# Performance work log

Hardware: AMD Instinct MI355X
Metric: run time of the kernel (lower is better)

The kernel has to match this reference:

```python
import jax, jax.numpy as jnp
import numpy as np

NPOINT, NSAMPLE, RADIUS = 2048, 32, 0.2
EPS = 1e-5


def setup_inputs() -> dict:
    key = jax.random.key(0)
    ks = jax.random.split(key, 12)
    B, N, C = 8, 8192, 64
    mlp = [64, 64, 128]
    inp = {
        "xyz": jax.random.normal(ks[0], (B, 3, N), dtype=jnp.float32),
        "points": jax.random.normal(ks[1], (B, C, N), dtype=jnp.float32),
    }
    last = C + 3  # use_xyz concatenates 3 relative coords
    for i, out in enumerate(mlp, 1):
        inp[f"W{i}"] = jax.random.normal(ks[2 * i], (out, last), dtype=jnp.float32) / np.sqrt(last).astype(np.float32)
        inp[f"b{i}"] = jnp.zeros((out,), jnp.float32)
        inp[f"g{i}"] = jnp.ones((out,), jnp.float32)
        inp[f"be{i}"] = jnp.zeros((out,), jnp.float32)
        last = out
    return inp


def fps(xyz_t, npoint):
    """Farthest point sampling. xyz_t: (B,N,3) -> (B,npoint) int32 indices."""
    xyz_t = jax.lax.stop_gradient(xyz_t)  # indices are non-differentiable
    B, N, _ = xyz_t.shape

    def step(carry, _):
        dists, far = carry  # (B,N), (B,)
        cent = jnp.take_along_axis(xyz_t, far[:, None, None], axis=1)  # (B,1,3)
        d = jnp.sum((xyz_t - cent) ** 2, axis=-1)
        dists = jnp.minimum(dists, d)
        nf = jnp.argmax(dists, axis=-1).astype(jnp.int32)
        return (dists, nf), far

    init = (jnp.full((B, N), 1e10, xyz_t.dtype), jnp.zeros((B,), jnp.int32))
    _, idxs = jax.lax.scan(step, init, None, length=npoint)
    return jnp.transpose(idxs)  # (B, npoint)


def ball_query(xyz_t, new_xyz_t, radius, nsample):
    """First-nsample-in-radius neighbor indices, padded with first hit.
    xyz_t (B,N,3), new_xyz_t (B,M,3) -> (B,M,nsample) int32."""
    B, N, _ = xyz_t.shape
    # squared distances via gemm to avoid (B,M,N,3) intermediate
    sq = (jnp.sum(new_xyz_t ** 2, -1)[:, :, None]
          + jnp.sum(xyz_t ** 2, -1)[:, None, :]
          - 2.0 * jnp.einsum('bmd,bnd->bmn', new_xyz_t, xyz_t))  # (B,M,N)
    cand = jnp.where(sq < radius * radius, jnp.arange(N, dtype=jnp.int32), N)
    idx = jnp.sort(cand, axis=-1)[:, :, :nsample]  # first k in-radius by index order
    first = idx[:, :, :1]
    first = jnp.where(first == N, 0, first)  # guard empty groups
    idx = jnp.where(idx == N, first, idx)
    return idx


def group(feat, idx):
    """feat (B,C,N), idx (B,M,k) -> (B,C,M,k) gathered neighbor features."""
    return jnp.take_along_axis(feat[:, :, None, :], idx[:, None, :, :], axis=3)


def conv_bn_relu(x, W, b, g, be):
    """Shared 1x1 Conv2d + BatchNorm2d (batch stats, training mode) + ReLU.
    x: (B,C,M,K) -> (B,O,M,K)."""
    y = jnp.einsum('oc,bcmk->bomk', W, x) + b[None, :, None, None]
    mu = jnp.mean(y, axis=(0, 2, 3), keepdims=True)
    var = jnp.var(y, axis=(0, 2, 3), keepdims=True)
    y = (y - mu) * jax.lax.rsqrt(var + EPS)
    y = y * g[None, :, None, None] + be[None, :, None, None]
    return jax.nn.relu(y)


def reference(xyz, points, W1, b1, g1, be1, W2, b2, g2, be2, W3, b3, g3, be3):
    xyz_t = jnp.transpose(xyz, (0, 2, 1))  # (B,N,3)
    fidx = fps(xyz_t, NPOINT)  # (B,M)
    new_xyz = jnp.take_along_axis(xyz, fidx[:, None, :], axis=2)  # (B,3,M)
    idx = ball_query(xyz_t, jnp.transpose(new_xyz, (0, 2, 1)), RADIUS, NSAMPLE)  # (B,M,K)
    grouped_xyz = group(xyz, idx) - new_xyz[:, :, :, None]  # (B,3,M,K) centered
    grouped_pts = group(points, idx)  # (B,f,M,K)
    x = jnp.concatenate([grouped_xyz, grouped_pts], axis=1)  # (B,f+3,M,K)
    x = conv_bn_relu(x, W1, b1, g1, be1)
    x = conv_bn_relu(x, W2, b2, g2, be2)
    x = conv_bn_relu(x, W3, b3, g3, be3)
    new_points = jnp.max(x, axis=3)  # (B,mlp[-1],M)
    return (new_xyz, new_points)
```

## Files before the change

### kernel.cpp

```cpp
#include <hip/hip_runtime.h>

#define BB 8
#define NN 8192
#define MM 2048
#define KK 32
#define NTOT (BB*MM*KK)

#define WS_PTS_T  0
#define WS_XYZN   4194304
#define WS_IDX    5242880
#define WS_GPART  5767168
#define WS_PARAMS 6291456
#define WS_ZMAX   6292480
#define WS_ZMIN   8389632
#define WS_TOTAL  10486784

typedef float v2f __attribute__((ext_vector_type(2)));

__global__ __launch_bounds__(256) void k_transpose(const float* __restrict__ pts,
                                                   float* __restrict__ pts_t){
  __shared__ float tile[64][65];
  int bid = blockIdx.x;
  int b = bid >> 7;
  int n0 = (bid & 127) << 6;
  int tx = threadIdx.x & 63, ty = threadIdx.x >> 6;
  const float* src = pts + (size_t)b*64*NN;
  #pragma unroll
  for (int c = ty; c < 64; c += 4)
    tile[c][tx] = src[(size_t)c*NN + n0 + tx];
  __syncthreads();
  float* dst = pts_t + ((size_t)b*NN + n0)*64;
  #pragma unroll
  for (int r = ty; r < 64; r += 4)
    dst[(size_t)r*64 + tx] = tile[tx][r];
}

__global__ __launch_bounds__(256) void k_xyzn(const float* __restrict__ xyz,
                                              float4* __restrict__ xyzn){
  #pragma clang fp contract(off)
  int i = blockIdx.x*256 + threadIdx.x;
  int b = i >> 13, n = i & 8191;
  const float* p = xyz + (size_t)b*3*NN;
  float x = p[n], y = p[NN+n], z = p[2*NN+n];
  float nrm = (x*x + y*y) + z*z;
  xyzn[i] = make_float4(x, y, z, nrm);
}

#define FPS_DPP_STEP(ctrl, rmask)                                            \
  {                                                                          \
    unsigned int lo_ = (unsigned int)key, hi_ = (unsigned int)(key >> 32);   \
    unsigned int sl_ = (unsigned int)__builtin_amdgcn_update_dpp(            \
        (int)lo_, (int)lo_, (ctrl), (rmask), 0xf, false);                    \
    unsigned int sh_ = (unsigned int)__builtin_amdgcn_update_dpp(            \
        (int)hi_, (int)hi_, (ctrl), (rmask), 0xf, false);                    \
    unsigned long long ok_ = ((unsigned long long)sh_ << 32) | sl_;          \
    if (ok_ > key) key = ok_;                                                \
  }

__global__ __launch_bounds__(512,1) void k_fps(const float* __restrict__ xyz,
                                               float* __restrict__ out_newxyz){
  #pragma clang fp contract(off)
  __shared__ float4 sp4[NN];
  __shared__ unsigned long long swk[2][8];
  int b = blockIdx.x, tid = threadIdx.x;
  const float* xb = xyz + (size_t)b*3*NN;
  int n0 = tid << 4;
  v2f px[8], py[8], pz[8], dd[8];
  const float4* xb4 = (const float4*)xb;
  #pragma unroll
  for (int q = 0; q < 4; ++q){
    float4 X = xb4[(n0>>2) + q];
    float4 Y = xb4[(NN>>2) + (n0>>2) + q];
    float4 Z = xb4[((2*NN)>>2) + (n0>>2) + q];
    px[2*q]   = (v2f){X.x, X.y}; px[2*q+1] = (v2f){X.z, X.w};
    py[2*q]   = (v2f){Y.x, Y.y}; py[2*q+1] = (v2f){Y.z, Y.w};
    pz[2*q]   = (v2f){Z.x, Z.y}; pz[2*q+1] = (v2f){Z.z, Z.w};
    dd[2*q]   = (v2f){1e10f,1e10f}; dd[2*q+1] = (v2f){1e10f,1e10f};
    sp4[n0+4*q+0] = make_float4(X.x, Y.x, Z.x, 0.f);
    sp4[n0+4*q+1] = make_float4(X.y, Y.y, Z.y, 0.f);
    sp4[n0+4*q+2] = make_float4(X.z, Y.z, Z.z, 0.f);
    sp4[n0+4*q+3] = make_float4(X.w, Y.w, Z.w, 0.f);
  }
  __syncthreads();
  float4 c0 = sp4[0];
  float cx = c0.x, cy = c0.y, cz = c0.z;
  float* ob = out_newxyz + (size_t)b*3*MM;
  int lane = tid & 63, wid = tid >> 6;
  for (int s = 0; s < 4; ++s){
    float ox = 0.f, oy = 0.f, oz = 0.f;
    for (int ti = 0; ti < 512; ++ti){
      if (tid == ti){ ox = cx; oy = cy; oz = cz; }
      v2f cvx = (v2f){cx,cx}, cvy = (v2f){cy,cy}, cvz = (v2f){cz,cz};
      v2f bv2 = (v2f){-1.f,-1.f};
      #pragma unroll
      for (int g = 0; g < 8; ++g){
        v2f dx = px[g]-cvx, dy = py[g]-cvy, dz = pz[g]-cvz;
        v2f xx = dx*dx, yy = dy*dy, zz = dz*dz;
        v2f sum = xx + yy;
        v2f d = sum + zz;
        v2f nd = __builtin_elementwise_min(dd[g], d);
        dd[g] = nd;
        bv2 = __builtin_elementwise_max(bv2, nd);
      }
      float bv = fmaxf(bv2.x, bv2.y);
      int bj = 0;
      #pragma unroll
      for (int g = 7; g >= 0; --g){
        if (dd[g].y == bv) bj = 2*g+1;
        if (dd[g].x == bv) bj = 2*g;
      }
      unsigned int n = (unsigned int)(n0 + bj);
      unsigned long long key =
          ((unsigned long long)__float_as_uint(bv) << 32) | (unsigned int)(~n);
      FPS_DPP_STEP(0x111, 0xf)
      FPS_DPP_STEP(0x112, 0xf)
      FPS_DPP_STEP(0x114, 0xf)
      FPS_DPP_STEP(0x118, 0xf)
      FPS_DPP_STEP(0x142, 0xa)
      FPS_DPP_STEP(0x143, 0xc)
      int buf = ti & 1;
      if (lane == 63) swk[buf][wid] = key;
      __syncthreads();
      const unsigned long long* kk = swk[buf];
      unsigned long long k0=kk[0], k1=kk[1], k2=kk[2], k3=kk[3];
      unsigned long long k4=kk[4], k5=kk[5], k6=kk[6], k7=kk[7];
      unsigned long long a = (k0>k1)?k0:k1, c = (k2>k3)?k2:k3;
      unsigned long long e = (k4>k5)?k4:k5, f = (k6>k7)?k6:k7;
      unsigned long long g2 = (a>c)?a:c,   h2 = (e>f)?e:f;
      unsigned long long kmax = (g2>h2)?g2:h2;
      int far = (int)(~(unsigned int)kmax) & (NN-1);
      float4 c4 = sp4[far];
      cx = c4.x; cy = c4.y; cz = c4.z;
    }
    ob[(s<<9)+tid] = ox; ob[MM+(s<<9)+tid] = oy; ob[2*MM+(s<<9)+tid] = oz;
  }
}

__global__ __launch_bounds__(256) void k_ballq(const float4* __restrict__ xyzn,
                                               const float* __restrict__ newxyz,
                                               int* __restrict__ idx){
  #pragma clang fp contract(off)
  __shared__ unsigned long long s_mask[32][129];
  __shared__ float4 s_c4[32];
  const float R2 = (float)(0.2*0.2);
  int b = blockIdx.x >> 6;
  int m0 = (blockIdx.x & 63) << 5;
  int tid = threadIdx.x, lane = tid & 63, wv = tid >> 6;
  const float* nb = newxyz + (size_t)b*3*MM;
  if (tid < 32){
    int m = m0 + tid;
    float cx = nb[m], cy = nb[MM+m], cz = nb[2*MM+m];
    float cn = (cx*cx + cy*cy) + cz*cz;
    s_c4[tid] = make_float4(cx, cy, cz, cn);
  }
  __syncthreads();
  const float4* src = xyzn + (size_t)b*NN;
  for (int ci = 0; ci < 32; ++ci){
    int ch = ci*4 + wv;
    float4 p = src[ch*64 + lane];
    #pragma unroll 8
    for (int mi = 0; mi < 32; ++mi){
      float4 c = s_c4[mi];
      float dot = (c.x*p.x + c.y*p.y) + c.z*p.z;
      float sq = (c.w + p.w) - 2.0f*dot;
      unsigned long long mk = __ballot(sq < R2);
      if (lane == 0) s_mask[mi][ch] = mk;
    }
  }
  __syncthreads();
  if (tid < 32){
    int m = m0 + tid;
    int* om = idx + ((size_t)(b*MM + m))*KK;
    int filled = 0, first = -1;
    for (int ch = 0; ch < 128 && filled < KK; ++ch){
      unsigned long long mk = s_mask[tid][ch];
      while (mk){
        int bp = __builtin_ctzll(mk);
        mk &= mk - 1;
        int j = ch*64 + bp;
        if (first < 0) first = j;
        om[filled++] = j;
        if (filled == KK) break;
      }
    }
    int pad = (first < 0) ? 0 : first;
    for (int s = filled; s < KK; ++s) om[s] = pad;
  }
}

#define XST 260

__device__ __forceinline__ void fma_po(float4& a0, float4& a1, float w,
                                       const float4& xA, const float4& xB){
  a0.x = fmaf(w, xA.x, a0.x); a0.y = fmaf(w, xA.y, a0.y);
  a0.z = fmaf(w, xA.z, a0.z); a0.w = fmaf(w, xA.w, a0.w);
  a1.x = fmaf(w, xB.x, a1.x); a1.y = fmaf(w, xB.y, a1.y);
  a1.z = fmaf(w, xB.z, a1.z); a1.w = fmaf(w, xB.w, a1.w);
}

__device__ __forceinline__ void gemm_step(float4 (&acc)[8][2], const float* sw,
                                          const float* sx, int c, int ob8, int pb){
  float4 xA = *(const float4*)&sx[c*XST + pb];
  float4 xB = *(const float4*)&sx[c*XST + pb + 4];
  float4 wA = *(const float4*)&sw[c*64 + ob8];
  float4 wB = *(const float4*)&sw[c*64 + ob8 + 4];
  fma_po(acc[0][0], acc[0][1], wA.x, xA, xB);
  fma_po(acc[1][0], acc[1][1], wA.y, xA, xB);
  fma_po(acc[2][0], acc[2][1], wA.z, xA, xB);
  fma_po(acc[3][0], acc[3][1], wA.w, xA, xB);
  fma_po(acc[4][0], acc[4][1], wB.x, xA, xB);
  fma_po(acc[5][0], acc[5][1], wB.y, xA, xB);
  fma_po(acc[6][0], acc[6][1], wB.z, xA, xB);
  fma_po(acc[7][0], acc[7][1], wB.w, xA, xB);
}

__device__ __forceinline__ void gather_col(float* sx, const float* pts_t,
    const float4* xyzn, const float* nb, const int* idx, int b, int bid, int tid){
  int m0 = (bid & 255) << 3;
  int m = m0 + (tid >> 5), k = tid & 31;
  int j = idx[((size_t)(b*MM + m))*KK + k];
  float4 P = xyzn[(size_t)b*NN + j];
  sx[0*XST + tid] = P.x - nb[m];
  sx[1*XST + tid] = P.y - nb[MM+m];
  sx[2*XST + tid] = P.z - nb[2*MM+m];
  const float4* pf = (const float4*)(pts_t + ((size_t)b*NN + j)*64);
  #pragma unroll
  for (int c4 = 0; c4 < 16; ++c4){
    float4 v = pf[c4];
    sx[(3+4*c4+0)*XST + tid] = v.x;
    sx[(3+4*c4+1)*XST + tid] = v.y;
    sx[(3+4*c4+2)*XST + tid] = v.z;
    sx[(3+4*c4+3)*XST + tid] = v.w;
  }
}

__device__ __forceinline__ void tile_stats(const float4 (&acc)[8][2], float* s_pp,
    float* gpart, int ob8, int pg, int tid, int bid, int nch_base){
  #pragma unroll
  for (int oi = 0; oi < 8; ++oi){
    float4 a0 = acc[oi][0], a1 = acc[oi][1];
    float s  = ((a0.x+a0.y)+(a0.z+a0.w)) + ((a1.x+a1.y)+(a1.z+a1.w));
    float q2 = ((a0.x*a0.x + a0.y*a0.y) + (a0.z*a0.z + a0.w*a0.w))
             + ((a1.x*a1.x + a1.y*a1.y) + (a1.z*a1.z + a1.w*a1.w));
    int o = ob8 + oi;
    s_pp[o*64 + pg*2 + 0] = s;
    s_pp[o*64 + pg*2 + 1] = q2;
  }
  __syncthreads();
  if (tid < 128){
    int o = tid >> 1, st = tid & 1;
    float S = 0.f;
    #pragma unroll 8
    for (int q = 0; q < 32; ++q) S += s_pp[o*64 + q*2 + st];
    gpart[(size_t)(st*128 + nch_base + o)*2048 + bid] = S;
  }
}

__global__ __launch_bounds__(256,1) void k_conv1_stats(const float* __restrict__ pts_t,
    const float4* __restrict__ xyzn, const float* __restrict__ newxyz,
    const int* __restrict__ idx, const float* __restrict__ W1, float* __restrict__ gpart){
  __shared__ float s_w1[67*64];
  __shared__ float s_x[67*XST];
  int tid = threadIdx.x;
  for (int i = tid; i < 67*64; i += 256){ int c = i>>6, o = i&63; s_w1[i] = W1[o*67 + c]; }
  int bid = blockIdx.x, b = bid >> 8;
  const float* nb = newxyz + (size_t)b*3*MM;
  gather_col(s_x, pts_t, xyzn, nb, idx, b, bid, tid);
  __syncthreads();
  int oq = tid & 7, pg = tid >> 3;
  int ob8 = oq*8, pb = pg*8;
  float4 acc[8][2];
  #pragma unroll
  for (int oi=0;oi<8;++oi){ acc[oi][0]=make_float4(0,0,0,0); acc[oi][1]=make_float4(0,0,0,0); }
  for (int c = 0; c < 67; ++c) gemm_step(acc, s_w1, s_x, c, ob8, pb);
  __syncthreads();
  tile_stats(acc, s_x, gpart, ob8, pg, tid, bid, 0);
}

__global__ __launch_bounds__(256,1) void k_conv2_stats(const float* __restrict__ pts_t,
    const float4* __restrict__ xyzn, const float* __restrict__ newxyz,
    const int* __restrict__ idx, const float* __restrict__ W1, const float* __restrict__ W2,
    const float* __restrict__ params1, float* __restrict__ gpart){
  __shared__ float s_w1[67*64];
  __shared__ float s_w2[64*64];
  __shared__ float s_p[128];
  __shared__ float s_x[67*XST];
  int tid = threadIdx.x;
  for (int i = tid; i < 67*64; i += 256){ int c = i>>6, o = i&63; s_w1[i] = W1[o*67 + c]; }
  for (int i = tid; i < 64*64; i += 256){ int c = i>>6, o = i&63; s_w2[i] = W2[o*64 + c]; }
  if (tid < 64){ s_p[tid] = params1[tid]; s_p[64+tid] = params1[128+tid]; }
  int bid = blockIdx.x, b = bid >> 8;
  const float* nb = newxyz + (size_t)b*3*MM;
  gather_col(s_x, pts_t, xyzn, nb, idx, b, bid, tid);
  __syncthreads();
  int oq = tid & 7, pg = tid >> 3;
  int ob8 = oq*8, pb = pg*8;
  float4 acc[8][2];
  #pragma unroll
  for (int oi=0;oi<8;++oi){ acc[oi][0]=make_float4(0,0,0,0); acc[oi][1]=make_float4(0,0,0,0); }
  for (int c = 0; c < 67; ++c) gemm_step(acc, s_w1, s_x, c, ob8, pb);
  float4 hreg[8][2];
  #pragma unroll
  for (int oi = 0; oi < 8; ++oi){
    float A = s_p[ob8+oi], C = s_p[64+ob8+oi];
    float4 z0 = acc[oi][0], z1 = acc[oi][1], h0, h1;
    h0.x = fmaxf(fmaf(A, z0.x, C), 0.f); h0.y = fmaxf(fmaf(A, z0.y, C), 0.f);
    h0.z = fmaxf(fmaf(A, z0.z, C), 0.f); h0.w = fmaxf(fmaf(A, z0.w, C), 0.f);
    h1.x = fmaxf(fmaf(A, z1.x, C), 0.f); h1.y = fmaxf(fmaf(A, z1.y, C), 0.f);
    h1.z = fmaxf(fmaf(A, z1.z, C), 0.f); h1.w = fmaxf(fmaf(A, z1.w, C), 0.f);
    hreg[oi][0] = h0; hreg[oi][1] = h1;
  }
  __syncthreads();
  #pragma unroll
  for (int oi = 0; oi < 8; ++oi){
    *(float4*)&s_x[(ob8+oi)*XST + pb]     = hreg[oi][0];
    *(float4*)&s_x[(ob8+oi)*XST + pb + 4] = hreg[oi][1];
  }
  __syncthreads();
  #pragma unroll
  for (int oi=0;oi<8;++oi){ acc[oi][0]=make_float4(0,0,0,0); acc[oi][1]=make_float4(0,0,0,0); }
  for (int c = 0; c < 64; ++c) gemm_step(acc, s_w2, s_x, c, ob8, pb);
  __syncthreads();
  tile_stats(acc, s_x, gpart, ob8, pg, tid, bid, 0);
}

__device__ __forceinline__ void accum_ch(float4* acc, const float4* w4, int c, float v){
  #pragma unroll
  for (int o4 = 0; o4 < 16; ++o4){
    float4 w = w4[c*16 + o4];
    acc[o4].x = fmaf(w.x, v, acc[o4].x);
    acc[o4].y = fmaf(w.y, v, acc[o4].y);
    acc[o4].z = fmaf(w.z, v, acc[o4].z);
    acc[o4].w = fmaf(w.w, v, acc[o4].w);
  }
}

__device__ __forceinline__ void conv1_pos(float4* acc, const float* s_w1,
    const float* pts_t, const float4* xyzn, const float* nb, int b, int m, int j){
  #pragma unroll
  for (int o4 = 0; o4 < 16; ++o4) acc[o4] = make_float4(0.f,0.f,0.f,0.f);
  float4 P = xyzn[(size_t)b*NN + j];
  float x0 = P.x - nb[m], x1 = P.y - nb[MM+m], x2 = P.z - nb[2*MM+m];
  const float4* w4 = (const float4*)s_w1;
  accum_ch(acc, w4, 0, x0);
  accum_ch(acc, w4, 1, x1);
  accum_ch(acc, w4, 2, x2);
  const float4* pf = (const float4*)(pts_t + ((size_t)b*NN + j)*64);
  #pragma unroll
  for (int c4 = 0; c4 < 16; ++c4){
    float4 v = pf[c4];
    accum_ch(acc, w4, 3+4*c4+0, v.x);
    accum_ch(acc, w4, 3+4*c4+1, v.y);
    accum_ch(acc, w4, 3+4*c4+2, v.z);
    accum_ch(acc, w4, 3+4*c4+3, v.w);
  }
}

__global__ __launch_bounds__(256) void k_bnfin(const float* __restrict__ gpart,
    const float* __restrict__ g, const float* __restrict__ be, float* __restrict__ params){
  int o = blockIdx.x, t = threadIdx.x;
  double s = 0.0, sq = 0.0;
  for (int i = t; i < 2048; i += 256){
    s  += (double)gpart[(size_t)o*2048 + i];
    sq += (double)gpart[(size_t)(128+o)*2048 + i];
  }
  __shared__ double ds[256], dq[256];
  ds[t] = s; dq[t] = sq; __syncthreads();
  for (int off = 128; off > 0; off >>= 1){
    if (t < off){ ds[t] += ds[t+off]; dq[t] += dq[t+off]; }
    __syncthreads();
  }
  if (t == 0){
    double mu = ds[0] / (double)NTOT;
    double var = dq[0] / (double)NTOT - mu*mu;
    float A = g[o] / sqrtf((float)var + 1e-5f);
    float Cc = be[o] - (float)mu * A;
    params[o] = A; params[128+o] = Cc;
  }
}

__global__ __launch_bounds__(256,1) void k_conv3(const float* __restrict__ pts_t,
    const float4* __restrict__ xyzn, const float* __restrict__ newxyz,
    const int* __restrict__ idx, const float* __restrict__ W1, const float* __restrict__ W2,
    const float* __restrict__ W3, const float* __restrict__ params1,
    const float* __restrict__ params2, float* __restrict__ gpart,
    float* __restrict__ zmax, float* __restrict__ zmin){
  __shared__ float s_w1[67*64];
  __shared__ float s_w2[64*64];
  __shared__ float s_p[256];
  __shared__ float s_z[256*68];
  __shared__ float s_sm[8*128*2];
  int tid = threadIdx.x;
  for (int i = tid; i < 67*64; i += 256){ int c = i>>6, o = i&63; s_w1[i] = W1[o*67 + c]; }
  for (int i = tid; i < 64*64; i += 256){ int c = i>>6, o = i&63; s_w2[i] = W2[o*64 + c]; }
  if (tid < 64){
    s_p[tid]      = params1[tid];     s_p[64+tid]  = params1[128+tid];
    s_p[128+tid]  = params2[tid];     s_p[192+tid] = params2[128+tid];
  }
  __syncthreads();
  int bid = blockIdx.x, b = bid >> 8, m0 = (bid & 255) << 3;
  {
    int m = m0 + (tid >> 5), k = tid & 31;
    int j = idx[((size_t)(b*MM + m))*KK + k];
    const float* nb = newxyz + (size_t)b*3*MM;
    float4 acc[16];
    conv1_pos(acc, s_w1, pts_t, xyzn, nb, b, m, j);
    float4 h[16];
    #pragma unroll
    for (int o4 = 0; o4 < 16; ++o4){
      float4 z = acc[o4], hh;
      hh.x = fmaxf(fmaf(s_p[4*o4+0], z.x, s_p[64+4*o4+0]), 0.f);
      hh.y = fmaxf(fmaf(s_p[4*o4+1], z.y, s_p[64+4*o4+1]), 0.f);
      hh.z = fmaxf(fmaf(s_p[4*o4+2], z.z, s_p[64+4*o4+2]), 0.f);
      hh.w = fmaxf(fmaf(s_p[4*o4+3], z.w, s_p[64+4*o4+3]), 0.f);
      h[o4] = hh;
    }
    float4 a2[16];
    #pragma unroll
    for (int o4 = 0; o4 < 16; ++o4) a2[o4] = make_float4(0.f,0.f,0.f,0.f);
    const float4* w24 = (const float4*)s_w2;
    #pragma unroll
    for (int c4 = 0; c4 < 16; ++c4){
      accum_ch(a2, w24, 4*c4+0, h[c4].x);
      accum_ch(a2, w24, 4*c4+1, h[c4].y);
      accum_ch(a2, w24, 4*c4+2, h[c4].z);
      accum_ch(a2, w24, 4*c4+3, h[c4].w);
    }
    #pragma unroll
    for (int o4 = 0; o4 < 16; ++o4){
      float4 z = a2[o4], hh;
      hh.x = fmaxf(fmaf(s_p[128+4*o4+0], z.x, s_p[192+4*o4+0]), 0.f);
      hh.y = fmaxf(fmaf(s_p[128+4*o4+1], z.y, s_p[192+4*o4+1]), 0.f);
      hh.z = fmaxf(fmaf(s_p[128+4*o4+2], z.z, s_p[192+4*o4+2]), 0.f);
      hh.w = fmaxf(fmaf(s_p[128+4*o4+3], z.w, s_p[192+4*o4+3]), 0.f);
      *(float4*)&s_z[tid*68 + o4*4] = hh;
    }
  }
  __syncthreads();
  int ml = tid >> 5, og = tid & 31;
  float accK[4][32];
  #pragma unroll
  for (int oo = 0; oo < 4; ++oo)
    #pragma unroll
    for (int k2 = 0; k2 < 32; ++k2) accK[oo][k2] = 0.f;
  const float4* w3g = (const float4*)W3;
  #pragma unroll
  for (int c4 = 0; c4 < 16; ++c4){
    float4 w[4];
    #pragma unroll
    for (int oo = 0; oo < 4; ++oo) w[oo] = w3g[(og*4+oo)*16 + c4];
    #pragma unroll
    for (int k2 = 0; k2 < 32; ++k2){
      float4 hv = *(const float4*)&s_z[(ml*32+k2)*68 + c4*4];
      #pragma unroll
      for (int oo = 0; oo < 4; ++oo){
        accK[oo][k2] = fmaf(w[oo].x, hv.x, accK[oo][k2]);
        accK[oo][k2] = fmaf(w[oo].y, hv.y, accK[oo][k2]);
        accK[oo][k2] = fmaf(w[oo].z, hv.z, accK[oo][k2]);
        accK[oo][k2] = fmaf(w[oo].w, hv.w, accK[oo][k2]);
      }
    }
  }
  int m = m0 + ml;
  #pragma unroll
  for (int oo = 0; oo < 4; ++oo){
    float mx = -3.4e38f, mn = 3.4e38f, s = 0.f, sq = 0.f;
    #pragma unroll
    for (int k2 = 0; k2 < 32; ++k2){
      float v = accK[oo][k2];
      mx = fmaxf(mx, v); mn = fminf(mn, v);
      s += v; sq = fmaf(v, v, sq);
    }
    int o = og*4 + oo;
    zmax[((size_t)(b*128 + o))*MM + m] = mx;
    zmin[((size_t)(b*128 + o))*MM + m] = mn;
    s_sm[(ml*128+o)*2] = s; s_sm[(ml*128+o)*2+1] = sq;
  }
  __syncthreads();
  {
    int o = tid >> 1, st = tid & 1;
    float S = 0.f;
    #pragma unroll
    for (int mm = 0; mm < 8; ++mm) S += s_sm[(mm*128+o)*2 + st];
    gpart[(size_t)(st*128+o)*2048 + bid] = S;
  }
}

__global__ __launch_bounds__(256) void k_out(const float* __restrict__ zmax,
    const float* __restrict__ zmin, const float* __restrict__ params3,
    float* __restrict__ out){
  int i = blockIdx.x*256 + threadIdx.x;
  int o = (i >> 11) & 127;
  float A = params3[o], Cc = params3[128+o];
  float v = (A >= 0.f) ? fmaf(A, zmax[i], Cc) : fmaf(A, zmin[i], Cc);
  out[49152 + i] = fmaxf(v, 0.f);
}

extern "C" void kernel_launch(void* const* d_in, const int* in_sizes, int n_in,
                              void* d_out, int out_size, void* d_ws, size_t ws_size,
                              hipStream_t stream){
  const float* xyz    = (const float*)d_in[0];
  const float* points = (const float*)d_in[1];
  const float* W1  = (const float*)d_in[2];
  const float* g1  = (const float*)d_in[4];
  const float* be1 = (const float*)d_in[5];
  const float* W2  = (const float*)d_in[6];
  const float* g2  = (const float*)d_in[8];
  const float* be2 = (const float*)d_in[9];
  const float* W3  = (const float*)d_in[10];
  const float* g3  = (const float*)d_in[12];
  const float* be3 = (const float*)d_in[13];

  if (ws_size < (size_t)WS_TOTAL * sizeof(float)) return;

  float*  ws     = (float*)d_ws;
  float*  pts_t  = ws + WS_PTS_T;
  float4* xyzn   = (float4*)(ws + WS_XYZN);
  int*    idx    = (int*)(ws + WS_IDX);
  float*  gpart  = ws + WS_GPART;
  float*  params = ws + WS_PARAMS;
  float*  zmax   = ws + WS_ZMAX;
  float*  zmin   = ws + WS_ZMIN;
  float*  out    = (float*)d_out;
  float*  newxyz = out;

  hipLaunchKernelGGL(k_fps,       dim3(8),    dim3(512), 0, stream, xyz, newxyz);
  hipLaunchKernelGGL(k_transpose, dim3(1024), dim3(256), 0, stream, points, pts_t);
  hipLaunchKernelGGL(k_xyzn,      dim3(256),  dim3(256), 0, stream, xyz, xyzn);
  hipLaunchKernelGGL(k_ballq,     dim3(512),  dim3(256), 0, stream, xyzn, newxyz, idx);
  hipLaunchKernelGGL(k_conv1_stats, dim3(2048), dim3(256), 0, stream,
                     pts_t, xyzn, newxyz, idx, W1, gpart);
  hipLaunchKernelGGL(k_bnfin, dim3(64), dim3(256), 0, stream, gpart, g1, be1, params+0);
  hipLaunchKernelGGL(k_conv2_stats, dim3(2048), dim3(256), 0, stream,
                     pts_t, xyzn, newxyz, idx, W1, W2, params+0, gpart);
  hipLaunchKernelGGL(k_bnfin, dim3(64), dim3(256), 0, stream, gpart, g2, be2, params+256);
  hipLaunchKernelGGL(k_conv3, dim3(2048), dim3(256), 0, stream,
                     pts_t, xyzn, newxyz, idx, W1, W2, W3, params+0, params+256,
                     gpart, zmax, zmin);
  hipLaunchKernelGGL(k_bnfin, dim3(128), dim3(256), 0, stream, gpart, g3, be3, params+512);
  hipLaunchKernelGGL(k_out, dim3(8192), dim3(256), 0, stream, zmax, zmin, params+512, out);
}
```

Baseline: 2.895 ms.

## Halve FPS block size, reduce float max via DPP then ballot for index

The FPS kernel now runs 256 threads per batch instead of 512, so each thread holds 32 points and the cross-wave reduction covers only 4 waves. The wave-level argmax does a 32-bit float max over DPP, then recovers the winning lane with ballot and readlane, replacing the 64-bit packed key reduction. It also pads the stats scratch stride to 66 to avoid LDS bank conflicts. This trades more per-thread work and registers for cheaper reductions and barriers on the serial FPS critical path. Tie-breaking should still pick the lowest index, since lanes hold ascending index ranges.

```diff
diff --git a/kernel.cpp b/kernel.cpp
--- a/kernel.cpp
+++ b/kernel.cpp
@@ -46,29 +46,25 @@
   xyzn[i] = make_float4(x, y, z, nrm);
 }
 
-#define FPS_DPP_STEP(ctrl, rmask)                                            \
+#define DPPMAXF(ctrl, rmask)                                                 \
   {                                                                          \
-    unsigned int lo_ = (unsigned int)key, hi_ = (unsigned int)(key >> 32);   \
-    unsigned int sl_ = (unsigned int)__builtin_amdgcn_update_dpp(            \
-        (int)lo_, (int)lo_, (ctrl), (rmask), 0xf, false);                    \
-    unsigned int sh_ = (unsigned int)__builtin_amdgcn_update_dpp(            \
-        (int)hi_, (int)hi_, (ctrl), (rmask), 0xf, false);                    \
-    unsigned long long ok_ = ((unsigned long long)sh_ << 32) | sl_;          \
-    if (ok_ > key) key = ok_;                                                \
-  }
-
-__global__ __launch_bounds__(512,1) void k_fps(const float* __restrict__ xyz,
+    float s_ = __int_as_float(__builtin_amdgcn_update_dpp(                   \
+        __float_as_int(m), __float_as_int(m), (ctrl), (rmask), 0xf, false)); \
+    m = fmaxf(m, s_);                                                        \
+  }
+
+__global__ __launch_bounds__(256,1) void k_fps(const float* __restrict__ xyz,
                                                float* __restrict__ out_newxyz){
   #pragma clang fp contract(off)
   __shared__ float4 sp4[NN];
-  __shared__ unsigned long long swk[2][8];
+  __shared__ unsigned long long swk[2][4];
   int b = blockIdx.x, tid = threadIdx.x;
   const float* xb = xyz + (size_t)b*3*NN;
-  int n0 = tid << 4;
-  v2f px[8], py[8], pz[8], dd[8];
+  int n0 = tid << 5;
+  v2f px[16], py[16], pz[16], dd[16];
   const float4* xb4 = (const float4*)xb;
   #pragma unroll
-  for (int q = 0; q < 4; ++q){
+  for (int q = 0; q < 8; ++q){
     float4 X = xb4[(n0>>2) + q];
     float4 Y = xb4[(NN>>2) + (n0>>2) + q];
     float4 Z = xb4[((2*NN)>>2) + (n0>>2) + q];
@@ -86,53 +82,58 @@
   float cx = c0.x, cy = c0.y, cz = c0.z;
   float* ob = out_newxyz + (size_t)b*3*MM;
   int lane = tid & 63, wid = tid >> 6;
-  for (int s = 0; s < 4; ++s){
+  for (int s = 0; s < 8; ++s){
     float ox = 0.f, oy = 0.f, oz = 0.f;
-    for (int ti = 0; ti < 512; ++ti){
+    #pragma unroll 1
+    for (int ti = 0; ti < 256; ++ti){
       if (tid == ti){ ox = cx; oy = cy; oz = cz; }
       v2f cvx = (v2f){cx,cx}, cvy = (v2f){cy,cy}, cvz = (v2f){cz,cz};
       v2f bv2 = (v2f){-1.f,-1.f};
       #pragma unroll
-      for (int g = 0; g < 8; ++g){
+      for (int g = 0; g < 16; ++g){
         v2f dx = px[g]-cvx, dy = py[g]-cvy, dz = pz[g]-cvz;
         v2f xx = dx*dx, yy = dy*dy, zz = dz*dz;
-        v2f sum = xx + yy;
-        v2f d = sum + zz;
+        v2f sm = xx + yy;
+        v2f d  = sm + zz;
         v2f nd = __builtin_elementwise_min(dd[g], d);
         dd[g] = nd;
         bv2 = __builtin_elementwise_max(bv2, nd);
       }
       float bv = fmaxf(bv2.x, bv2.y);
+      float m = bv;
+      DPPMAXF(0x111, 0xf)
+      DPPMAXF(0x112, 0xf)
+      DPPMAXF(0x114, 0xf)
+      DPPMAXF(0x118, 0xf)
+      DPPMAXF(0x142, 0xa)
+      DPPMAXF(0x143, 0xc)
+      float wm = __int_as_float(__builtin_amdgcn_readlane(__float_as_int(m), 63));
+      unsigned long long msk = __ballot(bv == wm);
+      int wl = (int)__builtin_ctzll(msk);
       int bj = 0;
       #pragma unroll
-      for (int g = 7; g >= 0; --g){
+      for (int g = 15; g >= 0; --g){
         if (dd[g].y == bv) bj = 2*g+1;
         if (dd[g].x == bv) bj = 2*g;
       }
-      unsigned int n = (unsigned int)(n0 + bj);
-      unsigned long long key =
-          ((unsigned long long)__float_as_uint(bv) << 32) | (unsigned int)(~n);
-      FPS_DPP_STEP(0x111, 0xf)
-      FPS_DPP_STEP(0x112, 0xf)
-      FPS_DPP_STEP(0x114, 0xf)
-      FPS_DPP_STEP(0x118, 0xf)
-      FPS_DPP_STEP(0x142, 0xa)
-      FPS_DPP_STEP(0x143, 0xc)
+      int nwin = __builtin_amdgcn_readlane(n0 + bj, wl);
       int buf = ti & 1;
-      if (lane == 63) swk[buf][wid] = key;
+      if (lane == 0){
+        unsigned long long key =
+            ((unsigned long long)__float_as_uint(wm) << 32) |
+            (unsigned int)(~(unsigned int)nwin);
+        swk[buf][wid] = key;
+      }
       __syncthreads();
       const unsigned long long* kk = swk[buf];
       unsigned long long k0=kk[0], k1=kk[1], k2=kk[2], k3=kk[3];
-      unsigned long long k4=kk[4], k5=kk[5], k6=kk[6], k7=kk[7];
-      unsigned long long a = (k0>k1)?k0:k1, c = (k2>k3)?k2:k3;
-      unsigned long long e = (k4>k5)?k4:k5, f = (k6>k7)?k6:k7;
-      unsigned long long g2 = (a>c)?a:c,   h2 = (e>f)?e:f;
-      unsigned long long kmax = (g2>h2)?g2:h2;
+      unsigned long long a = (k0>k1)?k0:k1, c2 = (k2>k3)?k2:k3;
+      unsigned long long kmax = (a>c2)?a:c2;
       int far = (int)(~(unsigned int)kmax) & (NN-1);
       float4 c4 = sp4[far];
       cx = c4.x; cy = c4.y; cz = c4.z;
     }
-    ob[(s<<9)+tid] = ox; ob[MM+(s<<9)+tid] = oy; ob[2*MM+(s<<9)+tid] = oz;
+    ob[(s<<8)+tid] = ox; ob[MM+(s<<8)+tid] = oy; ob[2*MM+(s<<8)+tid] = oz;
   }
 }
 
@@ -189,6 +190,7 @@
 }
 
 #define XST 260
+#define PST 66
 
 __device__ __forceinline__ void fma_po(float4& a0, float4& a1, float w,
                                        const float4& xA, const float4& xB){
@@ -243,15 +245,15 @@
     float q2 = ((a0.x*a0.x + a0.y*a0.y) + (a0.z*a0.z + a0.w*a0.w))
              + ((a1.x*a1.x + a1.y*a1.y) + (a1.z*a1.z + a1.w*a1.w));
     int o = ob8 + oi;
-    s_pp[o*64 + pg*2 + 0] = s;
-    s_pp[o*64 + pg*2 + 1] = q2;
+    s_pp[o*PST + pg*2 + 0] = s;
+    s_pp[o*PST + pg*2 + 1] = q2;
   }
   __syncthreads();
   if (tid < 128){
     int o = tid >> 1, st = tid & 1;
     float S = 0.f;
     #pragma unroll 8
-    for (int q = 0; q < 32; ++q) S += s_pp[o*64 + q*2 + st];
+    for (int q = 0; q < 32; ++q) S += s_pp[o*PST + q*2 + st];
     gpart[(size_t)(st*128 + nch_base + o)*2048 + bid] = S;
   }
 }
@@ -524,7 +526,7 @@
   float*  out    = (float*)d_out;
   float*  newxyz = out;
 
-  hipLaunchKernelGGL(k_fps,       dim3(8),    dim3(512), 0, stream, xyz, newxyz);
+  hipLaunchKernelGGL(k_fps,       dim3(8),    dim3(256), 0, stream, xyz, newxyz);
   hipLaunchKernelGGL(k_transpose, dim3(1024), dim3(256), 0, stream, points, pts_t);
   hipLaunchKernelGGL(k_xyzn,      dim3(256),  dim3(256), 0, stream, xyz, xyzn);
   hipLaunchKernelGGL(k_ballq,     dim3(512),  dim3(256), 0, stream, xyzn, newxyz, idx);
```

Measured after the change: 2.792 ms. -3.5%, faster.
